# Optimization experiments

Measured on AMD Instinct MI355X. Metric: run time of the kernel, lower is better.

## Reference

```python
import jax, jax.numpy as jnp
import numpy as np

INPUT_DIM = 512
HIDDEN_DIM = 256
REP_DIM = 256
SCORE_HIDDEN = 128


def setup_inputs() -> dict:
    key = jax.random.key(0)
    ks = jax.random.split(key, 12)
    def rn(k, shape, scale=None):
        s = scale if scale is not None else 1.0 / np.sqrt(shape[0])
        return jax.random.normal(k, shape, dtype=jnp.float32) * s
    return {
        "feat_x": jax.random.normal(ks[0], (512, INPUT_DIM), dtype=jnp.float32),
        "feat_pos": jax.random.normal(ks[1], (512, INPUT_DIM), dtype=jnp.float32),
        "feat_neg": jax.random.normal(ks[2], (512, INPUT_DIM), dtype=jnp.float32),
        # g: Linear(input,hidden) -> GELU -> Linear(hidden,rep); stored as x @ W
        "g_w1": rn(ks[3], (INPUT_DIM, HIDDEN_DIM)),
        "g_b1": jnp.zeros((HIDDEN_DIM,), jnp.float32),
        "g_w2": rn(ks[4], (HIDDEN_DIM, REP_DIM)),
        "g_b2": jnp.zeros((REP_DIM,), jnp.float32),
        # out_proj: Linear(rep, input, bias=False)
        "out_w": rn(ks[5], (REP_DIM, INPUT_DIM)),
        # score_net: Linear(3*rep+1, score_hidden) -> GELU -> Linear(score_hidden, 1)
        "s_w1": rn(ks[6], (3 * REP_DIM + 1, SCORE_HIDDEN)),
        "s_b1": jnp.zeros((SCORE_HIDDEN,), jnp.float32),
        "s_w2": rn(ks[7], (SCORE_HIDDEN, 1)),
        "s_b2": jnp.zeros((1,), jnp.float32),
    }


def _gelu(x):
    return jax.nn.gelu(x, approximate=False)  # torch nn.GELU default = exact erf


def _g(x, g_w1, g_b1, g_w2, g_b2):
    return _gelu(x @ g_w1 + g_b1) @ g_w2 + g_b2


def _set_operator(feat_x, feat_set, params):
    g_w1, g_b1, g_w2, g_b2, out_w, s_w1, s_b1, s_w2, s_b2 = params
    x_rep = _g(feat_x, g_w1, g_b1, g_w2, g_b2)   # (n, r)
    y_rep = _g(feat_set, g_w1, g_b1, g_w2, g_b2)  # (m, r)
    n, r = x_rep.shape
    m = y_rep.shape[0]
    x_exp = jnp.broadcast_to(x_rep[:, None, :], (n, m, r))
    y_exp = jnp.broadcast_to(y_rep[None, :, :], (n, m, r))
    delta = y_exp - x_exp                                   # (n, m, r)
    delta_norm = jnp.linalg.norm(delta, axis=-1, keepdims=True)
    score_in = jnp.concatenate([x_exp, y_exp, delta, delta_norm], axis=-1)  # (n, m, 3r+1)
    logits = (_gelu(score_in @ s_w1 + s_b1) @ s_w2 + s_b2)[..., 0]          # (n, m)
    weights = jax.nn.softmax(logits, axis=1)
    set_update_rep = jnp.einsum("nm,nmr->nr", weights, delta)
    return set_update_rep @ out_w


def reference(feat_x, feat_pos, feat_neg, g_w1, g_b1, g_w2, g_b2, out_w, s_w1, s_b1, s_w2, s_b2):
    params = (g_w1, g_b1, g_w2, g_b2, out_w, s_w1, s_b1, s_w2, s_b2)
    s_pos = _set_operator(feat_x, feat_pos, params)
    s_neg = _set_operator(feat_x, feat_neg, params)  # mask_self_neg=False
    return s_pos - s_neg
```

## Files before the change

kernel.cpp:

```cpp
#include <hip/hip_runtime.h>
#include <math.h>

#define NN 512
#define IN 512
#define HD 256
#define RD 256
#define SH 128

__device__ __forceinline__ float gelu_fast(float x){
    const float z  = x * 0.70710678118654752f;
    const float az = fabsf(z);
    const float t  = __builtin_amdgcn_rcpf(fmaf(0.3275911f, az, 1.0f));
    float p = fmaf(1.061405429f, t, -1.453152027f);
    p = fmaf(p, t, 1.421413741f);
    p = fmaf(p, t, -0.284496736f);
    p = fmaf(p, t, 0.254829592f);
    p = p * t;
    const float e = __builtin_amdgcn_exp2f(z * z * -1.4426950408889634f);
    const float E = p * e;
    const float one_plus_erf = (x >= 0.0f) ? (2.0f - E) : E;
    return 0.5f * x * one_plus_erf;
}

__global__ __launch_bounds__(512) void k_rep(
    const float* __restrict__ fx, const float* __restrict__ fp, const float* __restrict__ fn,
    const float* __restrict__ w1, const float* __restrict__ b1,
    const float* __restrict__ w2, const float* __restrict__ b2,
    const float* __restrict__ s_w1, const float* __restrict__ s_w2,
    float* __restrict__ r_x, float* __restrict__ r_p, float* __restrict__ r_n,
    float* __restrict__ rT_p, float* __restrict__ rT_n,
    float* __restrict__ A_x, float* __restrict__ BT_p, float* __restrict__ BT_n,
    float* __restrict__ nx2, float* __restrict__ np2, float* __restrict__ nn2,
    float* __restrict__ pB_p, float* __restrict__ pB_n)
{
    __shared__ float xs[4][IN];
    __shared__ float ps[8][4][HD];
    __shared__ float hs[4][HD];
    __shared__ float rloc[4][RD];
    __shared__ float ab4[4][SH];
    const int t = threadIdx.x;
    const int mat = blockIdx.x >> 7;
    const int row0 = (blockIdx.x & 127) << 2;
    const float* src = (mat==0) ? fx : (mat==1) ? fp : fn;

    {
        const int j = t >> 7, c4 = (t & 127) << 2;
        *(float4*)&xs[j][c4] = *(const float4*)&src[(row0+j)*IN + c4];
    }
    __syncthreads();

    const int cg = t & 63, s = t >> 6;
    const int c0 = cg << 2;

    {
        float4 acc[4];
        #pragma unroll
        for (int j=0;j<4;j++) acc[j] = make_float4(0.f,0.f,0.f,0.f);
        const float* wp = w1 + (s*64)*HD + c0;
        #pragma unroll 8
        for (int ii=0; ii<64; ii++){
            float4 w = *(const float4*)wp; wp += HD;
            const int i = s*64 + ii;
            #pragma unroll
            for (int j=0;j<4;j++){
                const float xv = xs[j][i];
                acc[j].x = fmaf(xv, w.x, acc[j].x);
                acc[j].y = fmaf(xv, w.y, acc[j].y);
                acc[j].z = fmaf(xv, w.z, acc[j].z);
                acc[j].w = fmaf(xv, w.w, acc[j].w);
            }
        }
        #pragma unroll
        for (int j=0;j<4;j++) *(float4*)&ps[s][j][c0] = acc[j];
    }
    __syncthreads();

    #pragma unroll
    for (int rep=0; rep<2; rep++){
        const int idx = rep*512 + t;
        const int j = idx >> 8, c = idx & 255;
        float v = b1[c];
        #pragma unroll
        for (int ss=0; ss<8; ss++) v += ps[ss][j][c];
        hs[j][c] = gelu_fast(v);
    }
    __syncthreads();

    {
        float4 acc[4];
        #pragma unroll
        for (int j=0;j<4;j++) acc[j] = make_float4(0.f,0.f,0.f,0.f);
        const float* wp = w2 + (s*32)*RD + c0;
        #pragma unroll 8
        for (int ii=0; ii<32; ii++){
            float4 w = *(const float4*)wp; wp += RD;
            const int i = s*32 + ii;
            #pragma unroll
            for (int j=0;j<4;j++){
                const float xv = hs[j][i];
                acc[j].x = fmaf(xv, w.x, acc[j].x);
                acc[j].y = fmaf(xv, w.y, acc[j].y);
                acc[j].z = fmaf(xv, w.z, acc[j].z);
                acc[j].w = fmaf(xv, w.w, acc[j].w);
            }
        }
        #pragma unroll
        for (int j=0;j<4;j++) *(float4*)&ps[s][j][c0] = acc[j];
    }
    __syncthreads();

    float* rout = (mat==0) ? r_x : (mat==1) ? r_p : r_n;
    #pragma unroll
    for (int rep=0; rep<2; rep++){
        const int idx = rep*512 + t;
        const int j = idx >> 8, c = idx & 255;
        float v = b2[c];
        #pragma unroll
        for (int ss=0; ss<8; ss++) v += ps[ss][j][c];
        rloc[j][c] = v;
        rout[(row0+j)*RD + c] = v;
    }
    __syncthreads();

    if (t < 256){
        const int w = t >> 6, l = t & 63;
        float v = 0.f;
        #pragma unroll
        for (int q=0;q<4;q++){ const float e = rloc[w][l + 64*q]; v = fmaf(e,e,v); }
        #pragma unroll
        for (int off=32; off>=1; off>>=1) v += __shfl_xor(v, off);
        if (l==0){
            float* nrm = (mat==0) ? nx2 : (mat==1) ? np2 : nn2;
            nrm[row0 + w] = v;
        }
    }
    if (mat && t < 256){
        float* rT = (mat==1) ? rT_p : rT_n;
        float4 q = make_float4(rloc[0][t], rloc[1][t], rloc[2][t], rloc[3][t]);
        *(float4*)&rT[t*NN + row0] = q;
    }

    {
        const int cg2 = t & 31, s2 = t >> 5;
        const int cc0 = cg2 << 2;
        const float sgn = (mat==0) ? -1.0f : 1.0f;
        const int base1 = (mat==0) ? 0 : 256;
        const float* p1 = s_w1 + (base1 + s2*16)*SH + cc0;
        const float* p3 = s_w1 + (512   + s2*16)*SH + cc0;
        float4 a[4];
        #pragma unroll
        for (int j=0;j<4;j++) a[j] = make_float4(0.f,0.f,0.f,0.f);
        #pragma unroll 8
        for (int ii=0; ii<16; ii++){
            float4 wa = *(const float4*)p1; p1 += SH;
            float4 wd = *(const float4*)p3; p3 += SH;
            float4 w;
            w.x = fmaf(sgn, wd.x, wa.x);
            w.y = fmaf(sgn, wd.y, wa.y);
            w.z = fmaf(sgn, wd.z, wa.z);
            w.w = fmaf(sgn, wd.w, wa.w);
            const int i = s2*16 + ii;
            #pragma unroll
            for (int j=0;j<4;j++){
                const float xv = rloc[j][i];
                a[j].x = fmaf(xv, w.x, a[j].x);
                a[j].y = fmaf(xv, w.y, a[j].y);
                a[j].z = fmaf(xv, w.z, a[j].z);
                a[j].w = fmaf(xv, w.w, a[j].w);
            }
        }
        float* psf = &ps[0][0][0];
        #pragma unroll
        for (int j=0;j<4;j++) *(float4*)&psf[(s2*4 + j)*SH + cc0] = a[j];
    }
    __syncthreads();

    {
        const float* psf = &ps[0][0][0];
        const int j = t >> 7, c = t & 127;
        float v = 0.f;
        #pragma unroll
        for (int ss=0; ss<16; ss++) v += psf[(ss*4 + j)*SH + c];
        if (mat==0) A_x[(row0+j)*SH + c] = v;
        else        ab4[j][c] = v;
    }
    __syncthreads();
    if (mat && t < 128){
        float* BT = (mat==1) ? BT_p : BT_n;
        float4 q = make_float4(ab4[0][t], ab4[1][t], ab4[2][t], ab4[3][t]);
        *(float4*)&BT[t*NN + row0] = q;
    }
    if (mat && t < 256){
        const int w = t >> 6, l = t & 63;
        const float w2a = 0.5f * s_w2[l];
        const float w2b = 0.5f * s_w2[l + 64];
        float v = ab4[w][l]*w2a + ab4[w][l+64]*w2b;
        #pragma unroll
        for (int off=32; off>=1; off>>=1) v += __shfl_xor(v, off);
        if (l == 0){
            float* pB = (mat==1) ? pB_p : pB_n;
            pB[row0 + w] = v;
        }
    }
}

#define GELU_NL_ACC(dnv, cav, accv)                                              \
    {                                                                            \
        const float u  = fmaf(dnv, wk.x, cav + B);                               \
        const float au = fabsf(u);                                               \
        const float tt = __builtin_amdgcn_rcpf(fmaf(0.3326725f, au, 1.0f));      \
        const float P  = fmaf(fmaf(0.7478556f, tt, -0.0958798f), tt, 0.3480242f) * tt; \
        const float e2 = __builtin_amdgcn_exp2f(u * u * -0.72134752044448170f);  \
        accv = fmaf(wk.y, fmaf(-au, P * e2, au), accv);                          \
    }

__global__ __launch_bounds__(256, 4) void k_sd(
    const float* __restrict__ r_x, const float* __restrict__ rT_p, const float* __restrict__ rT_n,
    const float* __restrict__ A_x, const float* __restrict__ BT_p, const float* __restrict__ BT_n,
    const float* __restrict__ r_p, const float* __restrict__ r_n,
    const float* __restrict__ nx2, const float* __restrict__ np2, const float* __restrict__ nn2,
    const float* __restrict__ pB_p, const float* __restrict__ pB_n,
    const float* __restrict__ s_w1, const float* __restrict__ s_b1,
    const float* __restrict__ s_w2,
    float* __restrict__ psum, float* __restrict__ Spart)
{
    __shared__ float4 xsA[RD];
    __shared__ float4 xsB[RD];
    __shared__ float4 cmA[SH];
    __shared__ float4 cmB[SH];
    __shared__ float2 cmW[SH];
    __shared__ float  pd[8][4][64];
    __shared__ float  ny2v[64];
    __shared__ __align__(16) float evb8[64][8];
    const int t = threadIdx.x;
    const int set = blockIdx.x >> 9;
    const int rem = blockIdx.x & 511;
    const int n0 = (rem >> 3) << 3;
    const int mt = rem & 7;
    const int mbase = mt << 6;
    const int tm = t & 63, kh = t >> 6;
    const int m = mbase + tm;
    const float* yT = set ? rT_n : rT_p;
    const float* BT = set ? BT_n : BT_p;

    const float nx0 = nx2[n0];
    const float nx1 = nx2[n0 + 1];
    const float nx2v = nx2[n0 + 2];
    const float nx3 = nx2[n0 + 3];
    const float nx4 = nx2[n0 + 4];
    const float nx5 = nx2[n0 + 5];
    const float nx6 = nx2[n0 + 6];
    const float nx7 = nx2[n0 + 7];
    const float pBm = (set ? pB_n : pB_p)[m];

    xsA[t] = make_float4(r_x[(n0+0)*RD + t], r_x[(n0+1)*RD + t],
                         r_x[(n0+2)*RD + t], r_x[(n0+3)*RD + t]);
    xsB[t] = make_float4(r_x[(n0+4)*RD + t], r_x[(n0+5)*RD + t],
                         r_x[(n0+6)*RD + t], r_x[(n0+7)*RD + t]);
    if (t < SH){
        const float b1v = s_b1[t];
        cmA[t] = make_float4(A_x[(n0+0)*SH + t] + b1v, A_x[(n0+1)*SH + t] + b1v,
                             A_x[(n0+2)*SH + t] + b1v, A_x[(n0+3)*SH + t] + b1v);
        cmB[t] = make_float4(A_x[(n0+4)*SH + t] + b1v, A_x[(n0+5)*SH + t] + b1v,
                             A_x[(n0+6)*SH + t] + b1v, A_x[(n0+7)*SH + t] + b1v);
        cmW[t] = make_float2(s_w1[768*SH + t], 0.5f * s_w2[t]);
    }
    if (t < 64) ny2v[t] = (set ? nn2 : np2)[mbase + t];
    __syncthreads();

    float pAk0, pAk1, c0;
    {
        const float4 aL = cmA[tm], aH = cmA[tm + 64];
        const float4 bL = cmB[tm], bH = cmB[tm + 64];
        const float2 wL = cmW[tm], wH = cmW[tm + 64];
        const float vaL = (kh==0)?aL.x:(kh==1)?aL.y:(kh==2)?aL.z:aL.w;
        const float vaH = (kh==0)?aH.x:(kh==1)?aH.y:(kh==2)?aH.z:aH.w;
        const float vbL = (kh==0)?bL.x:(kh==1)?bL.y:(kh==2)?bL.z:bL.w;
        const float vbH = (kh==0)?bH.x:(kh==1)?bH.y:(kh==2)?bH.z:bH.w;
        float p0 = vaL*wL.y + vaH*wH.y;
        float p1 = vbL*wL.y + vbH*wH.y;
        float cc = wL.x*wL.y + wH.x*wH.y;
        #pragma unroll
        for (int off=32; off>=1; off>>=1){
            p0 += __shfl_xor(p0, off);
            p1 += __shfl_xor(p1, off);
            cc += __shfl_xor(cc, off);
        }
        pAk0 = p0; pAk1 = p1; c0 = cc;
    }

    {
        float d0=0.f,d1=0.f,d2=0.f,d3=0.f,d4=0.f,d5=0.f,d6=0.f,d7=0.f;
        const float* yp = yT + (kh << 6)*NN + m;
        #pragma unroll 4
        for (int rr=0; rr<64; rr++){
            const float y = yp[rr*NN];
            const float4 xa = xsA[(kh << 6) + rr];
            const float4 xb = xsB[(kh << 6) + rr];
            d0 = fmaf(xa.x, y, d0); d1 = fmaf(xa.y, y, d1);
            d2 = fmaf(xa.z, y, d2); d3 = fmaf(xa.w, y, d3);
            d4 = fmaf(xb.x, y, d4); d5 = fmaf(xb.y, y, d5);
            d6 = fmaf(xb.z, y, d6); d7 = fmaf(xb.w, y, d7);
        }
        pd[0][kh][tm] = d0; pd[1][kh][tm] = d1;
        pd[2][kh][tm] = d2; pd[3][kh][tm] = d3;
        pd[4][kh][tm] = d4; pd[5][kh][tm] = d5;
        pd[6][kh][tm] = d6; pd[7][kh][tm] = d7;
    }
    __syncthreads();
    float dn0,dn1,dn2,dn3,dn4,dn5,dn6,dn7;
    {
        const float nyc = ny2v[tm];
        const float s0 = pd[0][0][tm]+pd[0][1][tm]+pd[0][2][tm]+pd[0][3][tm];
        const float s1 = pd[1][0][tm]+pd[1][1][tm]+pd[1][2][tm]+pd[1][3][tm];
        const float s2 = pd[2][0][tm]+pd[2][1][tm]+pd[2][2][tm]+pd[2][3][tm];
        const float s3 = pd[3][0][tm]+pd[3][1][tm]+pd[3][2][tm]+pd[3][3][tm];
        const float s4 = pd[4][0][tm]+pd[4][1][tm]+pd[4][2][tm]+pd[4][3][tm];
        const float s5 = pd[5][0][tm]+pd[5][1][tm]+pd[5][2][tm]+pd[5][3][tm];
        const float s6 = pd[6][0][tm]+pd[6][1][tm]+pd[6][2][tm]+pd[6][3][tm];
        const float s7 = pd[7][0][tm]+pd[7][1][tm]+pd[7][2][tm]+pd[7][3][tm];
        dn0 = sqrtf(fmaxf(fmaf(-2.f, s0, nx0  + nyc), 0.f));
        dn1 = sqrtf(fmaxf(fmaf(-2.f, s1, nx1  + nyc), 0.f));
        dn2 = sqrtf(fmaxf(fmaf(-2.f, s2, nx2v + nyc), 0.f));
        dn3 = sqrtf(fmaxf(fmaf(-2.f, s3, nx3  + nyc), 0.f));
        dn4 = sqrtf(fmaxf(fmaf(-2.f, s4, nx4  + nyc), 0.f));
        dn5 = sqrtf(fmaxf(fmaf(-2.f, s5, nx5  + nyc), 0.f));
        dn6 = sqrtf(fmaxf(fmaf(-2.f, s6, nx6  + nyc), 0.f));
        dn7 = sqrtf(fmaxf(fmaf(-2.f, s7, nx7  + nyc), 0.f));
    }

    float a0=0.f,a1=0.f,a2=0.f,a3=0.f,a4=0.f,a5=0.f,a6=0.f,a7=0.f;
    {
        const float* bp = BT + (kh << 5)*NN + m;
        #pragma unroll 2
        for (int kk=0; kk<32; kk++){
            const float  B  = bp[kk*NN];
            const float4 cA = cmA[(kh << 5) + kk];
            const float4 cB = cmB[(kh << 5) + kk];
            const float2 wk = cmW[(kh << 5) + kk];
            GELU_NL_ACC(dn0, cA.x, a0)
            GELU_NL_ACC(dn1, cA.y, a1)
            GELU_NL_ACC(dn2, cA.z, a2)
            GELU_NL_ACC(dn3, cA.w, a3)
            GELU_NL_ACC(dn4, cB.x, a4)
            GELU_NL_ACC(dn5, cB.y, a5)
            GELU_NL_ACC(dn6, cB.z, a6)
            GELU_NL_ACC(dn7, cB.w, a7)
        }
    }
    __syncthreads();
    pd[0][kh][tm] = a0; pd[1][kh][tm] = a1;
    pd[2][kh][tm] = a2; pd[3][kh][tm] = a3;
    pd[4][kh][tm] = a4; pd[5][kh][tm] = a5;
    pd[6][kh][tm] = a6; pd[7][kh][tm] = a7;
    __syncthreads();

    {
        const float L2E = 1.4426950408889634f;
        const float nlL = pd[kh  ][0][tm]+pd[kh  ][1][tm]+pd[kh  ][2][tm]+pd[kh  ][3][tm];
        const float nlH = pd[kh+4][0][tm]+pd[kh+4][1][tm]+pd[kh+4][2][tm]+pd[kh+4][3][tm];
        const float dnL = (kh==0)?dn0:(kh==1)?dn1:(kh==2)?dn2:dn3;
        const float dnH = (kh==0)?dn4:(kh==1)?dn5:(kh==2)?dn6:dn7;
        const float lgL = pAk0 + pBm + dnL*c0 + nlL;
        const float lgH = pAk1 + pBm + dnH*c0 + nlH;
        const float evL = __builtin_amdgcn_exp2f(lgL * L2E);
        const float evH = __builtin_amdgcn_exp2f(lgH * L2E);
        evb8[tm][kh]     = evL;
        evb8[tm][kh + 4] = evH;
        float vL = evL, vH = evH;
        #pragma unroll
        for (int off=32; off>=1; off>>=1){
            vL += __shfl_xor(vL, off);
            vH += __shfl_xor(vH, off);
        }
        if (tm == 0){
            float* Sp = Spart + (set*8 + mt)*NN + n0;
            Sp[kh]     = vL;
            Sp[kh + 4] = vH;
        }
    }
    __syncthreads();

    {
        const float* ry = (set ? r_n : r_p) + mbase*RD + t;
        float e0=0.f,e1=0.f,e2=0.f,e3=0.f,e4=0.f,e5=0.f,e6=0.f,e7=0.f;
        #pragma unroll 4
        for (int mm=0; mm<64; mm++){
            const float rv = ry[mm*RD];
            const float4 wlo = *(const float4*)&evb8[mm][0];
            const float4 whi = *(const float4*)&evb8[mm][4];
            e0 = fmaf(wlo.x, rv, e0); e1 = fmaf(wlo.y, rv, e1);
            e2 = fmaf(wlo.z, rv, e2); e3 = fmaf(wlo.w, rv, e3);
            e4 = fmaf(whi.x, rv, e4); e5 = fmaf(whi.y, rv, e5);
            e6 = fmaf(whi.z, rv, e6); e7 = fmaf(whi.w, rv, e7);
        }
        float* P = psum + ((set*8 + mt)*NN + n0)*RD;
        P[t]        = e0;
        P[RD + t]   = e1;
        P[2*RD + t] = e2;
        P[3*RD + t] = e3;
        P[4*RD + t] = e4;
        P[5*RD + t] = e5;
        P[6*RD + t] = e6;
        P[7*RD + t] = e7;
    }
}

__global__ __launch_bounds__(256) void k_fin(
    const float* __restrict__ psum, const float* __restrict__ Spart,
    const float* __restrict__ out_w, float* __restrict__ out)
{
    __shared__ float dv[2][RD];
    const int t = threadIdx.x;
    const int np = blockIdx.x >> 2, ct = blockIdx.x & 3;
    const int n0 = np << 1;
    const int cb = ct << 7;

    #pragma unroll
    for (int rep=0; rep<2; rep++){
        const int idx = rep*256 + t;
        const int j = idx >> 8, c = idx & 255;
        const int n = n0 + j;
        float Sp = 0.f, Sn = 0.f;
        #pragma unroll
        for (int q=0;q<8;q++){
            Sp += Spart[q*NN + n];
            Sn += Spart[(8+q)*NN + n];
        }
        float vp = 0.f, vn = 0.f;
        #pragma unroll
        for (int q=0;q<8;q++){
            vp += psum[(q*NN + n)*RD + c];
            vn += psum[((8+q)*NN + n)*RD + c];
        }
        dv[j][c] = vp * (1.0f/Sp) - vn * (1.0f/Sn);
    }
    __syncthreads();

    {
        const int j = t >> 7, cc = t & 127;
        const int col = cb + cc;
        float o = 0.f;
        const float* wo = out_w + col;
        #pragma unroll 8
        for (int r=0; r<RD; r++){ o = fmaf(dv[j][r], *wo, o); wo += IN; }
        out[(n0+j)*IN + col] = o;
    }
}

extern "C" void kernel_launch(void* const* d_in, const int* in_sizes, int n_in,
                              void* d_out, int out_size, void* d_ws, size_t ws_size,
                              hipStream_t stream)
{
    const float* fx  = (const float*)d_in[0];
    const float* fp  = (const float*)d_in[1];
    const float* fn  = (const float*)d_in[2];
    const float* gw1 = (const float*)d_in[3];
    const float* gb1 = (const float*)d_in[4];
    const float* gw2 = (const float*)d_in[5];
    const float* gb2 = (const float*)d_in[6];
    const float* ow  = (const float*)d_in[7];
    const float* sw1 = (const float*)d_in[8];
    const float* sb1 = (const float*)d_in[9];
    const float* sw2 = (const float*)d_in[10];
    float* out = (float*)d_out;

    float* ws   = (float*)d_ws;
    float* r_x  = ws;
    float* r_p  = r_x  + 131072;
    float* r_n  = r_p  + 131072;
    float* rT_p = r_n  + 131072;
    float* rT_n = rT_p + 131072;
    float* A_x  = rT_n + 131072;
    float* BT_p = A_x  + 65536;
    float* BT_n = BT_p + 65536;
    float* Spar = BT_n + 65536;
    float* nx2  = Spar + 8192;
    float* np2  = nx2  + 512;
    float* nn2  = np2  + 512;
    float* pB_p = nn2  + 512;
    float* pB_n = pB_p + 512;
    float* psum = pB_n + 512;

    hipLaunchKernelGGL(k_rep, dim3(384), dim3(512), 0, stream,
                       fx, fp, fn, gw1, gb1, gw2, gb2, sw1, sw2,
                       r_x, r_p, r_n, rT_p, rT_n, A_x, BT_p, BT_n,
                       nx2, np2, nn2, pB_p, pB_n);
    hipLaunchKernelGGL(k_sd, dim3(1024), dim3(256), 0, stream,
                       r_x, rT_p, rT_n, A_x, BT_p, BT_n, r_p, r_n,
                       nx2, np2, nn2, pB_p, pB_n, sw1, sb1, sw2, psum, Spar);
    hipLaunchKernelGGL(k_fin, dim3(1024), dim3(256), 0, stream,
                       psum, Spar, ow, out);
}
```

Baseline: 154.9 us.

## Double k_sd block to 512 threads, splitting reductions across eight k-slices

Launches the score kernel with 512 threads per block instead of 256. Each thread now handles half as many reduction steps in the dot-product and GELU-accumulation loops, using 8 k-slices instead of 4. Partial-sum staging in shared memory switches to float4 layouts, and the final weighted-sum stage splits its 8 rows across two thread halves. This aims to raise parallelism and latency hiding per block, at the cost of an extra barrier, more shared-memory reduction traffic, and launch bounds that demand 8 waves per SIMD, which may force register spills.

```diff
diff --git a/kernel.cpp b/kernel.cpp
--- a/kernel.cpp
+++ b/kernel.cpp
@@ -214,7 +214,7 @@
         accv = fmaf(wk.y, fmaf(-au, P * e2, au), accv);                          \
     }
 
-__global__ __launch_bounds__(256, 4) void k_sd(
+__global__ __launch_bounds__(512, 8) void k_sd(
     const float* __restrict__ r_x, const float* __restrict__ rT_p, const float* __restrict__ rT_n,
     const float* __restrict__ A_x, const float* __restrict__ BT_p, const float* __restrict__ BT_n,
     const float* __restrict__ r_p, const float* __restrict__ r_n,
@@ -229,7 +229,8 @@
     __shared__ float4 cmA[SH];
     __shared__ float4 cmB[SH];
     __shared__ float2 cmW[SH];
-    __shared__ float  pd[8][4][64];
+    __shared__ float4 pdA[8][64];
+    __shared__ float4 pdB[8][64];
     __shared__ float  ny2v[64];
     __shared__ __align__(16) float evb8[64][8];
     const int t = threadIdx.x;
@@ -243,101 +244,99 @@
     const float* yT = set ? rT_n : rT_p;
     const float* BT = set ? BT_n : BT_p;
 
-    const float nx0 = nx2[n0];
-    const float nx1 = nx2[n0 + 1];
-    const float nx2v = nx2[n0 + 2];
-    const float nx3 = nx2[n0 + 3];
-    const float nx4 = nx2[n0 + 4];
-    const float nx5 = nx2[n0 + 5];
-    const float nx6 = nx2[n0 + 6];
-    const float nx7 = nx2[n0 + 7];
     const float pBm = (set ? pB_n : pB_p)[m];
 
-    xsA[t] = make_float4(r_x[(n0+0)*RD + t], r_x[(n0+1)*RD + t],
-                         r_x[(n0+2)*RD + t], r_x[(n0+3)*RD + t]);
-    xsB[t] = make_float4(r_x[(n0+4)*RD + t], r_x[(n0+5)*RD + t],
-                         r_x[(n0+6)*RD + t], r_x[(n0+7)*RD + t]);
-    if (t < SH){
+    if (t < 256){
+        xsA[t] = make_float4(r_x[(n0+0)*RD + t], r_x[(n0+1)*RD + t],
+                             r_x[(n0+2)*RD + t], r_x[(n0+3)*RD + t]);
+    } else {
+        const int c = t - 256;
+        xsB[c] = make_float4(r_x[(n0+4)*RD + c], r_x[(n0+5)*RD + c],
+                             r_x[(n0+6)*RD + c], r_x[(n0+7)*RD + c]);
+    }
+    if (t < 128){
         const float b1v = s_b1[t];
         cmA[t] = make_float4(A_x[(n0+0)*SH + t] + b1v, A_x[(n0+1)*SH + t] + b1v,
                              A_x[(n0+2)*SH + t] + b1v, A_x[(n0+3)*SH + t] + b1v);
-        cmB[t] = make_float4(A_x[(n0+4)*SH + t] + b1v, A_x[(n0+5)*SH + t] + b1v,
-                             A_x[(n0+6)*SH + t] + b1v, A_x[(n0+7)*SH + t] + b1v);
         cmW[t] = make_float2(s_w1[768*SH + t], 0.5f * s_w2[t]);
+    } else if (t < 256){
+        const int c = t - 128;
+        const float b1v = s_b1[c];
+        cmB[c] = make_float4(A_x[(n0+4)*SH + c] + b1v, A_x[(n0+5)*SH + c] + b1v,
+                             A_x[(n0+6)*SH + c] + b1v, A_x[(n0+7)*SH + c] + b1v);
     }
     if (t < 64) ny2v[t] = (set ? nn2 : np2)[mbase + t];
     __syncthreads();
 
-    float pAk0, pAk1, c0;
-    {
-        const float4 aL = cmA[tm], aH = cmA[tm + 64];
-        const float4 bL = cmB[tm], bH = cmB[tm + 64];
+    float pAk, c0v;
+    {
         const float2 wL = cmW[tm], wH = cmW[tm + 64];
-        const float vaL = (kh==0)?aL.x:(kh==1)?aL.y:(kh==2)?aL.z:aL.w;
-        const float vaH = (kh==0)?aH.x:(kh==1)?aH.y:(kh==2)?aH.z:aH.w;
-        const float vbL = (kh==0)?bL.x:(kh==1)?bL.y:(kh==2)?bL.z:bL.w;
-        const float vbH = (kh==0)?bH.x:(kh==1)?bH.y:(kh==2)?bH.z:bH.w;
-        float p0 = vaL*wL.y + vaH*wH.y;
-        float p1 = vbL*wL.y + vbH*wH.y;
+        const float4 aL = (kh < 4) ? cmA[tm]      : cmB[tm];
+        const float4 aH = (kh < 4) ? cmA[tm + 64] : cmB[tm + 64];
+        const int kc = kh & 3;
+        const float vaL = (kc==0)?aL.x:(kc==1)?aL.y:(kc==2)?aL.z:aL.w;
+        const float vaH = (kc==0)?aH.x:(kc==1)?aH.y:(kc==2)?aH.z:aH.w;
+        float pa = vaL*wL.y + vaH*wH.y;
         float cc = wL.x*wL.y + wH.x*wH.y;
         #pragma unroll
         for (int off=32; off>=1; off>>=1){
-            p0 += __shfl_xor(p0, off);
-            p1 += __shfl_xor(p1, off);
+            pa += __shfl_xor(pa, off);
             cc += __shfl_xor(cc, off);
         }
-        pAk0 = p0; pAk1 = p1; c0 = cc;
+        pAk = pa; c0v = cc;
     }
 
     {
         float d0=0.f,d1=0.f,d2=0.f,d3=0.f,d4=0.f,d5=0.f,d6=0.f,d7=0.f;
-        const float* yp = yT + (kh << 6)*NN + m;
-        #pragma unroll 4
-        for (int rr=0; rr<64; rr++){
+        const int r0 = kh << 5;
+        const float* yp = yT + r0*NN + m;
+        #pragma unroll 8
+        for (int rr=0; rr<32; rr++){
             const float y = yp[rr*NN];
-            const float4 xa = xsA[(kh << 6) + rr];
-            const float4 xb = xsB[(kh << 6) + rr];
+            const float4 xa = xsA[r0 + rr];
+            const float4 xb = xsB[r0 + rr];
             d0 = fmaf(xa.x, y, d0); d1 = fmaf(xa.y, y, d1);
             d2 = fmaf(xa.z, y, d2); d3 = fmaf(xa.w, y, d3);
             d4 = fmaf(xb.x, y, d4); d5 = fmaf(xb.y, y, d5);
             d6 = fmaf(xb.z, y, d6); d7 = fmaf(xb.w, y, d7);
         }
-        pd[0][kh][tm] = d0; pd[1][kh][tm] = d1;
-        pd[2][kh][tm] = d2; pd[3][kh][tm] = d3;
-        pd[4][kh][tm] = d4; pd[5][kh][tm] = d5;
-        pd[6][kh][tm] = d6; pd[7][kh][tm] = d7;
-    }
-    __syncthreads();
+        pdA[kh][tm] = make_float4(d0, d1, d2, d3);
+        pdB[kh][tm] = make_float4(d4, d5, d6, d7);
+    }
+    __syncthreads();
+
     float dn0,dn1,dn2,dn3,dn4,dn5,dn6,dn7;
     {
+        float s0=0.f,s1=0.f,s2=0.f,s3=0.f,s4=0.f,s5=0.f,s6=0.f,s7=0.f;
+        #pragma unroll
+        for (int s=0; s<8; s++){
+            const float4 qa = pdA[s][tm];
+            const float4 qb = pdB[s][tm];
+            s0 += qa.x; s1 += qa.y; s2 += qa.z; s3 += qa.w;
+            s4 += qb.x; s5 += qb.y; s6 += qb.z; s7 += qb.w;
+        }
         const float nyc = ny2v[tm];
-        const float s0 = pd[0][0][tm]+pd[0][1][tm]+pd[0][2][tm]+pd[0][3][tm];
-        const float s1 = pd[1][0][tm]+pd[1][1][tm]+pd[1][2][tm]+pd[1][3][tm];
-        const float s2 = pd[2][0][tm]+pd[2][1][tm]+pd[2][2][tm]+pd[2][3][tm];
-        const float s3 = pd[3][0][tm]+pd[3][1][tm]+pd[3][2][tm]+pd[3][3][tm];
-        const float s4 = pd[4][0][tm]+pd[4][1][tm]+pd[4][2][tm]+pd[4][3][tm];
-        const float s5 = pd[5][0][tm]+pd[5][1][tm]+pd[5][2][tm]+pd[5][3][tm];
-        const float s6 = pd[6][0][tm]+pd[6][1][tm]+pd[6][2][tm]+pd[6][3][tm];
-        const float s7 = pd[7][0][tm]+pd[7][1][tm]+pd[7][2][tm]+pd[7][3][tm];
-        dn0 = sqrtf(fmaxf(fmaf(-2.f, s0, nx0  + nyc), 0.f));
-        dn1 = sqrtf(fmaxf(fmaf(-2.f, s1, nx1  + nyc), 0.f));
-        dn2 = sqrtf(fmaxf(fmaf(-2.f, s2, nx2v + nyc), 0.f));
-        dn3 = sqrtf(fmaxf(fmaf(-2.f, s3, nx3  + nyc), 0.f));
-        dn4 = sqrtf(fmaxf(fmaf(-2.f, s4, nx4  + nyc), 0.f));
-        dn5 = sqrtf(fmaxf(fmaf(-2.f, s5, nx5  + nyc), 0.f));
-        dn6 = sqrtf(fmaxf(fmaf(-2.f, s6, nx6  + nyc), 0.f));
-        dn7 = sqrtf(fmaxf(fmaf(-2.f, s7, nx7  + nyc), 0.f));
-    }
+        dn0 = sqrtf(fmaxf(fmaf(-2.f, s0, nx2[n0+0] + nyc), 0.f));
+        dn1 = sqrtf(fmaxf(fmaf(-2.f, s1, nx2[n0+1] + nyc), 0.f));
+        dn2 = sqrtf(fmaxf(fmaf(-2.f, s2, nx2[n0+2] + nyc), 0.f));
+        dn3 = sqrtf(fmaxf(fmaf(-2.f, s3, nx2[n0+3] + nyc), 0.f));
+        dn4 = sqrtf(fmaxf(fmaf(-2.f, s4, nx2[n0+4] + nyc), 0.f));
+        dn5 = sqrtf(fmaxf(fmaf(-2.f, s5, nx2[n0+5] + nyc), 0.f));
+        dn6 = sqrtf(fmaxf(fmaf(-2.f, s6, nx2[n0+6] + nyc), 0.f));
+        dn7 = sqrtf(fmaxf(fmaf(-2.f, s7, nx2[n0+7] + nyc), 0.f));
+    }
+    __syncthreads();
 
     float a0=0.f,a1=0.f,a2=0.f,a3=0.f,a4=0.f,a5=0.f,a6=0.f,a7=0.f;
     {
-        const float* bp = BT + (kh << 5)*NN + m;
+        const int k0 = kh << 4;
+        const float* bp = BT + k0*NN + m;
         #pragma unroll 2
-        for (int kk=0; kk<32; kk++){
+        for (int kk=0; kk<16; kk++){
             const float  B  = bp[kk*NN];
-            const float4 cA = cmA[(kh << 5) + kk];
-            const float4 cB = cmB[(kh << 5) + kk];
-            const float2 wk = cmW[(kh << 5) + kk];
+            const float4 cA = cmA[k0 + kk];
+            const float4 cB = cmB[k0 + kk];
+            const float2 wk = cmW[k0 + kk];
             GELU_NL_ACC(dn0, cA.x, a0)
             GELU_NL_ACC(dn1, cA.y, a1)
             GELU_NL_ACC(dn2, cA.z, a2)
@@ -348,61 +347,49 @@
             GELU_NL_ACC(dn7, cB.w, a7)
         }
     }
-    __syncthreads();
-    pd[0][kh][tm] = a0; pd[1][kh][tm] = a1;
-    pd[2][kh][tm] = a2; pd[3][kh][tm] = a3;
-    pd[4][kh][tm] = a4; pd[5][kh][tm] = a5;
-    pd[6][kh][tm] = a6; pd[7][kh][tm] = a7;
+    pdA[kh][tm] = make_float4(a0, a1, a2, a3);
+    pdB[kh][tm] = make_float4(a4, a5, a6, a7);
     __syncthreads();
 
     {
         const float L2E = 1.4426950408889634f;
-        const float nlL = pd[kh  ][0][tm]+pd[kh  ][1][tm]+pd[kh  ][2][tm]+pd[kh  ][3][tm];
-        const float nlH = pd[kh+4][0][tm]+pd[kh+4][1][tm]+pd[kh+4][2][tm]+pd[kh+4][3][tm];
-        const float dnL = (kh==0)?dn0:(kh==1)?dn1:(kh==2)?dn2:dn3;
-        const float dnH = (kh==0)?dn4:(kh==1)?dn5:(kh==2)?dn6:dn7;
-        const float lgL = pAk0 + pBm + dnL*c0 + nlL;
-        const float lgH = pAk1 + pBm + dnH*c0 + nlH;
-        const float evL = __builtin_amdgcn_exp2f(lgL * L2E);
-        const float evH = __builtin_amdgcn_exp2f(lgH * L2E);
-        evb8[tm][kh]     = evL;
-        evb8[tm][kh + 4] = evH;
-        float vL = evL, vH = evH;
-        #pragma unroll
-        for (int off=32; off>=1; off>>=1){
-            vL += __shfl_xor(vL, off);
-            vH += __shfl_xor(vH, off);
-        }
-        if (tm == 0){
-            float* Sp = Spart + (set*8 + mt)*NN + n0;
-            Sp[kh]     = vL;
-            Sp[kh + 4] = vH;
-        }
-    }
-    __syncthreads();
-
-    {
-        const float* ry = (set ? r_n : r_p) + mbase*RD + t;
-        float e0=0.f,e1=0.f,e2=0.f,e3=0.f,e4=0.f,e5=0.f,e6=0.f,e7=0.f;
-        #pragma unroll 4
+        const float* pdrow = (kh < 4) ? (const float*)&pdA[0][0]
+                                      : (const float*)&pdB[0][0];
+        const int kc = kh & 3;
+        float nl = 0.f;
+        #pragma unroll
+        for (int s=0; s<8; s++) nl += pdrow[(s*64 + tm)*4 + kc];
+        const float dnk = (kh==0)?dn0:(kh==1)?dn1:(kh==2)?dn2:(kh==3)?dn3:
+                          (kh==4)?dn4:(kh==5)?dn5:(kh==6)?dn6:dn7;
+        const float logit = pAk + pBm + dnk*c0v + nl;
+        const float ev = __builtin_amdgcn_exp2f(logit * L2E);
+        evb8[tm][kh] = ev;
+        float v = ev;
+        #pragma unroll
+        for (int off=32; off>=1; off>>=1) v += __shfl_xor(v, off);
+        if (tm == 0) Spart[(set*8 + mt)*NN + n0 + kh] = v;
+    }
+    __syncthreads();
+
+    {
+        const int c  = t & 255;
+        const int rh = (t >> 8) << 2;
+        const float* ry = (set ? r_n : r_p) + mbase*RD + c;
+        float e0=0.f, e1=0.f, e2=0.f, e3=0.f;
+        #pragma unroll 8
         for (int mm=0; mm<64; mm++){
             const float rv = ry[mm*RD];
-            const float4 wlo = *(const float4*)&evb8[mm][0];
-            const float4 whi = *(const float4*)&evb8[mm][4];
-            e0 = fmaf(wlo.x, rv, e0); e1 = fmaf(wlo.y, rv, e1);
-            e2 = fmaf(wlo.z, rv, e2); e3 = fmaf(wlo.w, rv, e3);
-            e4 = fmaf(whi.x, rv, e4); e5 = fmaf(whi.y, rv, e5);
-            e6 = fmaf(whi.z, rv, e6); e7 = fmaf(whi.w, rv, e7);
-        }
-        float* P = psum + ((set*8 + mt)*NN + n0)*RD;
-        P[t]        = e0;
-        P[RD + t]   = e1;
-        P[2*RD + t] = e2;
-        P[3*RD + t] = e3;
-        P[4*RD + t] = e4;
-        P[5*RD + t] = e5;
-        P[6*RD + t] = e6;
-        P[7*RD + t] = e7;
+            const float4 w = *(const float4*)&evb8[mm][rh];
+            e0 = fmaf(w.x, rv, e0);
+            e1 = fmaf(w.y, rv, e1);
+            e2 = fmaf(w.z, rv, e2);
+            e3 = fmaf(w.w, rv, e3);
+        }
+        float* P = psum + ((set*8 + mt)*NN + n0 + rh)*RD;
+        P[c]        = e0;
+        P[RD + c]   = e1;
+        P[2*RD + c] = e2;
+        P[3*RD + c] = e3;
     }
 }
 
@@ -486,7 +473,7 @@
                        fx, fp, fn, gw1, gb1, gw2, gb2, sw1, sw2,
                        r_x, r_p, r_n, rT_p, rT_n, A_x, BT_p, BT_n,
                        nx2, np2, nn2, pB_p, pB_n);
-    hipLaunchKernelGGL(k_sd, dim3(1024), dim3(256), 0, stream,
+    hipLaunchKernelGGL(k_sd, dim3(1024), dim3(512), 0, stream,
                        r_x, rT_p, rT_n, A_x, BT_p, BT_n, r_p, r_n,
                        nx2, np2, nn2, pB_p, pB_n, sw1, sb1, sw2, psum, Spar);
     hipLaunchKernelGGL(k_fin, dim3(1024), dim3(256), 0, stream,
```

Measured after the change: 158.6 us. 1.02x slower.
